# Kernel optimization log

Hardware: AMD Instinct MI355X
Metric: run time of the kernel (lower is better)

The kernel has to match this reference:

```python
import jax, jax.numpy as jnp
import numpy as np

B, N, C = 4, 32768, 64
D_IN = B * C          # 256 == in_channels * batch_size
D_MODEL = 256
HEADS = 2
NUM_EDGES = 4096
N_INC = 131072
EPS = 1e-5
NEG = 0.2


def _leaky(v):
    return jnp.where(v >= 0, v, NEG * v)


def _bn(v, g, b, m, var):  # BatchNorm1d, eval mode (running stats)
    return g * (v - m) * jax.lax.rsqrt(var + EPS) + b


def setup_inputs() -> dict:
    key = jax.random.key(0)
    ks = jax.random.split(key, 16)

    def lin_init(k, fan_in, shape):
        lim = 1.0 / np.sqrt(fan_in)
        return jax.random.uniform(k, shape, jnp.float32, -lim, lim)

    x = jax.random.normal(ks[0], (B, N, C), jnp.float32)
    row_n = jax.random.randint(ks[1], (N_INC,), 0, N, jnp.int32)
    row_e = jax.random.randint(ks[2], (N_INC,), 0, NUM_EDGES, jnp.int32)
    row_e = row_e.at[0].set(NUM_EDGES - 1)  # guarantee max edge id -> num_edges
    hyperedge_all = jnp.stack([row_n, row_e])

    return {
        "x": x,
        "hyperedge_all": hyperedge_all,
        # linear1: d_in -> d_model
        "W1": lin_init(ks[3], D_IN, (D_MODEL, D_IN)),
        "b1": lin_init(ks[4], D_IN, (D_MODEL,)),
        "bn1_g": 1.0 + 0.1 * jax.random.normal(ks[5], (D_MODEL,), jnp.float32),
        "bn1_b": 0.1 * jax.random.normal(ks[6], (D_MODEL,), jnp.float32),
        "bn1_m": 0.01 * jax.random.normal(ks[7], (D_MODEL,), jnp.float32),
        "bn1_v": jnp.ones((D_MODEL,), jnp.float32),
        # HypergraphConv lin: d_model -> heads*d_model (no bias); att: [heads, 2*d_model]
        "attW": lin_init(ks[8], D_MODEL, (HEADS * D_MODEL, D_MODEL)),
        "att": 0.1 * jax.random.normal(ks[9], (HEADS, 2 * D_MODEL), jnp.float32),
        "cb": 0.01 * jax.random.normal(ks[10], (D_MODEL,), jnp.float32),
        "bn2_g": 1.0 + 0.1 * jax.random.normal(ks[11], (D_MODEL,), jnp.float32),
        "bn2_b": 0.1 * jax.random.normal(ks[12], (D_MODEL,), jnp.float32),
        "bn2_m": 0.01 * jax.random.normal(ks[13], (D_MODEL,), jnp.float32),
        "bn2_v": jnp.ones((D_MODEL,), jnp.float32),
        # linear2: d_model -> d_in
        "W2": lin_init(ks[14], D_MODEL, (D_IN, D_MODEL)),
        "b2": lin_init(ks[15], D_MODEL, (D_IN,)),
        "ln_g": jnp.ones((C,), jnp.float32),
        "ln_b": jnp.zeros((C,), jnp.float32),
    }


def reference(x, hyperedge_all, W1, b1, bn1_g, bn1_b, bn1_m, bn1_v,
              attW, att, cb, bn2_g, bn2_b, bn2_m, bn2_v, W2, b2, ln_g, ln_b):
    src = x
    h = x.reshape(N, B * C)                               # [N, D_IN] (raw row-major reshape, as torch)
    h = _leaky(h @ W1.T + b1)                             # [N, D_MODEL]
    h = _bn(h, bn1_g, bn1_b, bn1_m, bn1_v)

    idx_n = hyperedge_all[0]                              # [I] node index per incidence
    idx_e = hyperedge_all[1]                              # [I] hyperedge index per incidence

    # hyperedge_attr = A^T h where A is the (0/1, duplicate-summed) incidence matrix
    eattr = jax.ops.segment_sum(h[idx_n], idx_e, NUM_EDGES)            # [E, D_MODEL]

    # --- HypergraphConv with attention, concat=False ---
    xh = (h @ attW.T).reshape(N, HEADS, D_MODEL)                       # [N, H, D]
    ea = (eattr @ attW.T).reshape(NUM_EDGES, HEADS, D_MODEL)           # [E, H, D]
    att_n, att_e = att[:, :D_MODEL], att[:, D_MODEL:]                  # [H, D] each
    sn = jnp.einsum('nhd,hd->nh', xh, att_n)                           # node score
    se = jnp.einsum('ehd,hd->eh', ea, att_e)                           # edge score
    alpha = _leaky(sn[idx_n] + se[idx_e])                              # [I, H]
    # segment softmax over destination nodes (PyG softmax(alpha, hyperedge_index[0]))
    amax = jax.ops.segment_max(alpha, idx_n, N)
    amax = jnp.where(jnp.isfinite(amax), amax, 0.0)
    ex = jnp.exp(alpha - amax[idx_n])
    denom = jax.ops.segment_sum(ex, idx_n, N)
    alpha = ex / (denom[idx_n] + 1e-16)                                # [I, H]

    ones_i = jnp.ones((N_INC,), h.dtype)
    deg_n = jax.ops.segment_sum(ones_i, idx_n, N)                      # D (hyperedge_weight = 1)
    Dinv = jnp.where(deg_n > 0, 1.0 / deg_n, 0.0)
    deg_e = jax.ops.segment_sum(ones_i, idx_e, NUM_EDGES)              # B
    Binv = jnp.where(deg_e > 0, 1.0 / deg_e, 0.0)

    # node -> edge: edge_out[e] = sum_inc B[e] * alpha * xh[n]
    m1 = Binv[idx_e][:, None, None] * alpha[:, :, None] * xh[idx_n]    # [I, H, D]
    edge_out = jax.ops.segment_sum(m1, idx_e, NUM_EDGES)               # [E, H, D]
    # edge -> node: node_out[n] = sum_inc D[n] * alpha * edge_out[e]
    m2 = Dinv[idx_n][:, None, None] * alpha[:, :, None] * edge_out[idx_e]
    node_out = jax.ops.segment_sum(m2, idx_n, N)                       # [N, H, D]
    x2 = node_out.mean(axis=1) + cb                                    # concat=False -> head mean + bias

    h = _bn(h + x2, bn2_g, bn2_b, bn2_m, bn2_v)
    h = _leaky(h @ W2.T + b2)                                          # [N, D_IN]

    y = src + h.reshape(B, N, C)                                       # residual (raw reshape back)
    mu = y.mean(-1, keepdims=True)                                     # LayerNorm over C
    var = jnp.mean((y - mu) ** 2, -1, keepdims=True)
    return ln_g * (y - mu) * jax.lax.rsqrt(var + EPS) + ln_b
```

## Files before the change

kernel.cpp:

```cpp
#include <hip/hip_runtime.h>

#define NN 32768
#define EE 4096
#define NI 131072
#define NEGS 0.2f
#define EPSV 1e-5f

typedef __bf16 bf16;
typedef __bf16 bf16x8 __attribute__((ext_vector_type(8)));
typedef __bf16 bf16x4 __attribute__((ext_vector_type(4)));
typedef float f32x4 __attribute__((ext_vector_type(4)));

#define AS1 __attribute__((address_space(1)))
#define AS3 __attribute__((address_space(3)))

__device__ __forceinline__ void gld16(const void* g, void* l) {
    __builtin_amdgcn_global_load_lds((const AS1 unsigned*)g, (AS3 unsigned*)l, 16, 0, 0);
}

__device__ __forceinline__ void stage_hl(const bf16* WH, const bf16* WL, bf16* sW,
                                         int buf, int kk, int wave, int lane) {
#pragma unroll
    for (int i = 0; i < 4; ++i) {
        size_t goff = (size_t)(wave*64 + lane)*256 + (size_t)kk*32 + i*8;
        size_t lb = (size_t)buf*16384 + (size_t)(i*256 + wave*64)*8;
        gld16(WH + goff, sW + lb);
        gld16(WL + goff, sW + 8192 + lb);
    }
}

__device__ __forceinline__ void stage_w(const bf16* WB, bf16* sW,
                                        int buf, int kk, int wave, int lane) {
#pragma unroll
    for (int i = 0; i < 4; ++i) {
        gld16(WB + (size_t)(wave*64 + lane)*256 + (size_t)kk*32 + i*8,
              sW + (size_t)buf*8192 + (size_t)(i*256 + wave*64)*8);
    }
}

constexpr size_t OFF_FLAGS = 0;
constexpr size_t OFF_W1F   = 32;
constexpr size_t OFF_WAF   = OFF_W1F + 65536;
constexpr size_t OFF_W2F   = OFF_WAF + 131072;
constexpr size_t OFF_SN    = OFF_W2F + 65536;
constexpr size_t OFF_SE    = OFF_SN + (size_t)NN*2;
constexpr size_t OFF_ALPHA = OFF_SE + (size_t)EE*2;
constexpr size_t OFF_DENOM = OFF_ALPHA + (size_t)NI*2;
constexpr size_t OFF_DEGN  = OFF_DENOM + (size_t)NN*2;
constexpr size_t OFF_DEGE  = OFF_DEGN + (size_t)NN;
constexpr size_t OFF_EATTR = OFF_DEGE + (size_t)EE;
constexpr size_t OFF_EOUT  = OFF_EATTR + (size_t)EE*256;
constexpr size_t OFF_H     = OFF_EOUT + (size_t)EE*512;
constexpr size_t OFF_WBA2  = OFF_H + (size_t)NN*256;
constexpr size_t OFF_WN    = OFF_WBA2 + 65536;
constexpr size_t OFF_WE    = OFF_WN + 512;
constexpr size_t OFF_ECOFF = OFF_WE + 512;
constexpr size_t OFF_ECURS = OFF_ECOFF + 4100;
constexpr size_t OFF_ECLIST= OFF_ECURS + (size_t)EE;
constexpr size_t WS_TOTAL  = OFF_ECLIST + (size_t)NI;

__device__ __forceinline__ float leaky(float v) { return v < 0.f ? NEGS * v : v; }

__device__ __forceinline__ float rdv(const void* p, size_t i, int f) {
    return f ? (float)((const bf16*)p)[i] : ((const float*)p)[i];
}

__device__ __forceinline__ void rd_idx(const void* p, int i, int mode, int& n, int& e) {
    if (mode == 0)      { n = ((const int*)p)[i];            e = ((const int*)p)[NI + i]; }
    else if (mode == 2) { n = ((const int*)p)[2*i];          e = ((const int*)p)[2*i + 1]; }
    else if (mode == 1) { n = (int)((const long long*)p)[i]; e = (int)((const long long*)p)[NI + i]; }
    else if (mode == 3) { n = (int)((const float*)p)[i];     e = (int)((const float*)p)[NI + i]; }
    else                { n = 0; e = 0; }
    if ((unsigned)n >= NN) n = 0;
    if ((unsigned)e >= EE) e = 0;
}

__global__ void detect_kernel(const void* p0, const void* p2, const void* p3, const void* p4,
                              const void* p5, const void* p6, const void* p7, const void* p8,
                              const void* p9, const void* p10, const void* p11, const void* p12,
                              const void* p13, const void* p14, const void* p15, const void* p16,
                              const void* p17, const void* p18, int* F) {
    __shared__ int cnt;
    int b = blockIdx.x, t = threadIdx.x;
    const void* ps[19] = {p0, nullptr, p2, p3, p4, p5, p6, p7, p8, p9, p10,
                          p11, p12, p13, p14, p15, p16, p17, p18};
    const int scan[19] = {2048, 0, 2048, 256, 256, 256, 256, 0, 2048, 1024,
                          256, 256, 256, 256, 0, 256, 256, 0, 0};
    if (b == 1)  { if (t == 0) { F[1] = 1; F[26] = 0; F[27] = 0; F[28] = 0; F[29] = 0; } return; }
    if (b == 18) { if (t == 0) F[18] = 1; return; }
    if (b == 7 || b == 14 || b == 17) {
        if (t == 0) F[b] = (*(const unsigned*)ps[b] == 0x3F803F80u) ? 1 : 0;
        return;
    }
    if (t == 0) cnt = 0;
    __syncthreads();
    int n = scan[b];
    int local = 0;
    for (int i = t; i < n; i += 256) {
        unsigned short u = ((const unsigned short*)ps[b])[i];
        if (((u >> 7) & 0xFFu) >= 0xC0u) local = 1;
    }
    if (local) atomicAdd(&cnt, 1);
    __syncthreads();
    if (t == 0) F[b] = (cnt == 0) ? 1 : 0;
}

__global__ void k_setflags(int* F) {
    if (threadIdx.x == 0) {
        F[25] = (!F[26]) ? 0 : (!F[28]) ? 2 : (!F[27]) ? 1 : (!F[29]) ? 3 : 99;
        int a = 1;
        const int ids[18] = {0,2,3,4,5,6,7,8,9,10,11,12,13,14,15,16,17,18};
        for (int k = 0; k < 18; ++k) a &= F[ids[k]];
        F[20] = a;
    }
}

__global__ void k_idxcheck(const void* p, int* F) {
    int i = blockIdx.x * 256 + threadIdx.x;
    const int*       p32 = (const int*)p;
    const long long* p64 = (const long long*)p;
    const float*     pf  = (const float*)p;
    int n0 = p32[i], e0 = p32[NI + i];
    if ((unsigned)n0 >= NN || (unsigned)e0 >= EE) atomicOr(&F[26], 1);
    int n2 = p32[2*i], e2 = p32[2*i + 1];
    if ((unsigned)n2 >= NN || (unsigned)e2 >= EE) atomicOr(&F[28], 1);
    long long n1 = p64[i], e1 = p64[NI + i];
    if (n1 < 0 || n1 >= NN || e1 < 0 || e1 >= EE) atomicOr(&F[27], 1);
    float nf = pf[i], ef = pf[NI + i];
    if (!(nf >= 0.f && nf < (float)NN && nf == floorf(nf)) ||
        !(ef >= 0.f && ef < (float)EE && ef == floorf(ef))) atomicOr(&F[29], 1);
}

__global__ void marker_kernel(float* OUT, int code) {
    size_t i = (size_t)blockIdx.x * 256 + threadIdx.x;
    OUT[i] = (i == 1) ? (float)code : 0.f;
}

__global__ void convb_kernel(const void* src, bf16* dst, const int* F, int fidx) {
    size_t i = ((size_t)blockIdx.x * 256 + threadIdx.x) * 4;
    if (F[fidx]) {
        *(bf16x4*)(dst + i) = *(const bf16x4*)((const bf16*)src + i);
    } else {
        f32x4 v = *(const f32x4*)((const float*)src + i);
        bf16x4 o;
        o[0] = (bf16)v[0]; o[1] = (bf16)v[1]; o[2] = (bf16)v[2]; o[3] = (bf16)v[3];
        *(bf16x4*)(dst + i) = o;
    }
}

__global__ void k_w1conv(const void* W1, const int* F, bf16* WH, bf16* WL) {
    size_t i = (size_t)blockIdx.x * 256 + threadIdx.x;
    float w = rdv(W1, i, F[2]);
    bf16 h = (bf16)w;
    WH[i] = h;
    WL[i] = (bf16)(w - (float)h);
}

__global__ void k_prep2(const void* g2, const void* be2, const void* m2, const void* v2,
                        const void* cb, const int* F, float* ST) {
    int k = threadIdx.x;
    float s = rdv(g2, k, F[11]) * rsqrtf(rdv(v2, k, F[14]) + EPSV);
    float t = s * (rdv(cb, k, F[10]) - rdv(m2, k, F[13])) + rdv(be2, k, F[12]);
    ST[k] = s; ST[256 + k] = t;
}

__global__ void k_w2conv(const void* W2, const void* b2, const float* ST, const int* F,
                         bf16* WH, bf16* WL, float* B2P) {
    __shared__ float sacc[4];
    int c = blockIdx.x, k = threadIdx.x;
    float w  = rdv(W2, (size_t)c*256 + k, F[15]);
    float sw = ST[k] * w;
    bf16 h = (bf16)sw;
    WH[(size_t)c*256 + k] = h;
    WL[(size_t)c*256 + k] = (bf16)(sw - (float)h);
    float p = ST[256 + k] * w;
#pragma unroll
    for (int m = 32; m >= 1; m >>= 1) p += __shfl_xor(p, m, 64);
    int lane = k & 63, wv = k >> 6;
    if (lane == 0) sacc[wv] = p;
    __syncthreads();
    if (k == 0) B2P[c] = rdv(b2, c, F[16]) + sacc[0] + sacc[1] + sacc[2] + sacc[3];
}

__global__ void k_fold(const void* attW, const void* att, const int* F,
                       float* WN, float* WE) {
    int c = threadIdx.x;
    int h = blockIdx.y;
    int d0 = blockIdx.x * 16;
    int faw = F[8], fat = F[9];
    float swn = 0.f, swe = 0.f;
#pragma unroll 4
    for (int dd = 0; dd < 16; ++dd) {
        int d = d0 + dd;
        float w = rdv(attW, (size_t)(h*256 + d)*256 + c, faw);
        swn += w * rdv(att, h*512 + d, fat);
        swe += w * rdv(att, h*512 + 256 + d, fat);
    }
    atomicAdd(&WN[h*256 + c], swn);
    atomicAdd(&WE[h*256 + c], swe);
}

__global__ void k_deg(const void* __restrict__ idx, float* __restrict__ DEGN,
                      float* __restrict__ DEGE, const int* __restrict__ F) {
    int i = blockIdx.x * 256 + threadIdx.x;
    int n, e; rd_idx(idx, i, F[25], n, e);
    atomicAdd(&DEGN[n], 1.f);
    atomicAdd(&DEGE[e], 1.f);
}

__global__ void scan_a(const float* __restrict__ DEG, int* __restrict__ BSUM) {
    __shared__ int ws[4];
    int b = blockIdx.x, t = threadIdx.x, lane = t & 63, wave = t >> 6;
    f32x4 v = *(const f32x4*)(DEG + ((size_t)b*256 + t)*4);
    int s = (int)v[0] + (int)v[1] + (int)v[2] + (int)v[3];
#pragma unroll
    for (int m = 32; m >= 1; m >>= 1) s += __shfl_xor(s, m, 64);
    if (lane == 0) ws[wave] = s;
    __syncthreads();
    if (t == 0) BSUM[b] = ws[0] + ws[1] + ws[2] + ws[3];
}

__global__ void scan_b2(int* BSN, int* BSE) {
    if (threadIdx.x == 0) { int run = 0; for (int i = 0; i < 32; ++i) { int s = BSN[i]; BSN[i] = run; run += s; } }
    if (threadIdx.x == 1) { int run = 0; for (int i = 0; i < 4;  ++i) { int s = BSE[i]; BSE[i] = run; run += s; } }
}

__global__ void scan_c(float* __restrict__ DEG, const int* __restrict__ BSUM,
                       int* __restrict__ OFF, int* __restrict__ CURS, int total) {
    __shared__ int ws[4];
    int b = blockIdx.x, t = threadIdx.x, lane = t & 63, wave = t >> 6;
    f32x4 v = *(const f32x4*)(DEG + ((size_t)b*256 + t)*4);
    int c0 = (int)v[0], c1 = (int)v[1], c2 = (int)v[2], c3 = (int)v[3];
    int s = c0 + c1 + c2 + c3;
    int p = s;
#pragma unroll
    for (int off = 1; off < 64; off <<= 1) {
        int u = __shfl_up(p, off, 64);
        if (lane >= off) p += u;
    }
    if (lane == 63) ws[wave] = p;
    __syncthreads();
    int wb = 0;
    for (int w = 0; w < wave; ++w) wb += ws[w];
    int run = BSUM[b] + wb + p - s;
    int i0 = (b*256 + t)*4;
    int cs[4] = {c0, c1, c2, c3};
#pragma unroll
    for (int j = 0; j < 4; ++j) {
        OFF[i0 + j] = run; CURS[i0 + j] = run; run += cs[j];
        DEG[i0 + j] = cs[j] > 0 ? 1.f / (float)cs[j] : 0.f;
    }
    if (i0 + 4 == total) OFF[total] = run;
}

__global__ __launch_bounds__(256) void k_h_mfma(const void* __restrict__ x,
                                                const bf16* __restrict__ WH,
                                                const bf16* __restrict__ WL,
                                                const void* b1, const void* g1, const void* be1,
                                                const void* m1, const void* v1,
                                                const float* __restrict__ WN,
                                                const int* __restrict__ F,
                                                float* __restrict__ H,
                                                float* __restrict__ SN) {
    __shared__ float sB[256], sA[256], sM[256], sBE[256], sWN0[256], sWN1[256];
    __shared__ __align__(16) bf16 sW[32768];
    int tid = threadIdx.x;
    {
        sB[tid]  = rdv(b1, tid, F[3]);
        sA[tid]  = rdv(g1, tid, F[4]) * rsqrtf(rdv(v1, tid, F[7]) + EPSV);
        sM[tid]  = rdv(m1, tid, F[6]);
        sBE[tid] = rdv(be1, tid, F[5]);
        sWN0[tid] = WN[tid];
        sWN1[tid] = WN[256 + tid];
    }
    int lane = tid & 63, wave = tid >> 6;
    int l15 = lane & 15, quad = lane >> 4;
    int row0 = (blockIdx.x * 4 + wave) * 16;
    int fx = F[0];
    const size_t abase = (size_t)(row0 + l15) * 256;
    f32x4 acc[16];
#pragma unroll
    for (int t = 0; t < 16; ++t) acc[t] = (f32x4){0.f, 0.f, 0.f, 0.f};
    stage_hl(WH, WL, sW, 0, 0, wave, lane);
    bf16x8 aNb; f32x4 aN0, aN1;
    if (fx) {
        aNb = *(const bf16x8*)((const bf16*)x + abase + quad*8);
    } else {
        aN0 = *(const f32x4*)((const float*)x + abase + quad*8);
        aN1 = *(const f32x4*)((const float*)x + abase + quad*8 + 4);
    }
    __syncthreads();
    int cur = 0;
    for (int kk = 0; kk < 8; ++kk) {
        if (kk < 7) stage_hl(WH, WL, sW, cur ^ 1, kk + 1, wave, lane);
        bf16x8 ah, al;
        if (fx) {
            ah = aNb;
            if (kk < 7) aNb = *(const bf16x8*)((const bf16*)x + abase + (kk+1)*32 + quad*8);
        } else {
            f32x4 a0 = aN0, a1 = aN1;
            if (kk < 7) {
                aN0 = *(const f32x4*)((const float*)x + abase + (kk+1)*32 + quad*8);
                aN1 = *(const f32x4*)((const float*)x + abase + (kk+1)*32 + quad*8 + 4);
            }
#pragma unroll
            for (int j = 0; j < 4; ++j) {
                bf16 h0 = (bf16)a0[j]; ah[j] = h0; al[j] = (bf16)(a0[j] - (float)h0);
                bf16 h1 = (bf16)a1[j]; ah[4+j] = h1; al[4+j] = (bf16)(a1[j] - (float)h1);
            }
        }
        const bf16* pH = sW + cur*16384 + quad*2048 + l15*8;
        const bf16* pL = pH + 8192;
#pragma unroll
        for (int t = 0; t < 16; ++t) {
            bf16x8 bh = *(const bf16x8*)(pH + t*128);
            bf16x8 bl = *(const bf16x8*)(pL + t*128);
            acc[t] = __builtin_amdgcn_mfma_f32_16x16x32_bf16(ah, bh, acc[t], 0, 0, 0);
            if (!fx) acc[t] = __builtin_amdgcn_mfma_f32_16x16x32_bf16(al, bh, acc[t], 0, 0, 0);
            acc[t] = __builtin_amdgcn_mfma_f32_16x16x32_bf16(ah, bl, acc[t], 0, 0, 0);
        }
        __syncthreads();
        cur ^= 1;
    }
    float p0[4] = {0.f, 0.f, 0.f, 0.f}, p1[4] = {0.f, 0.f, 0.f, 0.f};
#pragma unroll
    for (int t = 0; t < 16; ++t) {
        int cc = t*16 + l15;
        float A = sA[cc], Mv = sM[cc], BE = sBE[cc], Bv = sB[cc];
        float w0 = sWN0[cc], w1 = sWN1[cc];
#pragma unroll
        for (int r = 0; r < 4; ++r) {
            int rr = row0 + quad*4 + r;
            float v = leaky(acc[t][r] + Bv);
            float hv = A * (v - Mv) + BE;
            H[(size_t)rr*256 + cc] = hv;
            p0[r] += hv * w0;
            p1[r] += hv * w1;
        }
    }
#pragma unroll
    for (int r = 0; r < 4; ++r) {
#pragma unroll
        for (int m = 8; m >= 1; m >>= 1) {
            p0[r] += __shfl_xor(p0[r], m, 64);
            p1[r] += __shfl_xor(p1[r], m, 64);
        }
        if (l15 == 0) {
            int rr = row0 + quad*4 + r;
            SN[(size_t)rr*2]     = p0[r];
            SN[(size_t)rr*2 + 1] = p1[r];
        }
    }
}

__global__ __launch_bounds__(256) void k_eattrg(const int* __restrict__ COFF,
                                                const int* __restrict__ CLIST,
                                                const void* __restrict__ idx,
                                                const float* __restrict__ H,
                                                const float* __restrict__ WE,
                                                float* __restrict__ SE,
                                                const int* __restrict__ F) {
    __shared__ int s_n[128];
    __shared__ float sq0[4], sq1[4];
    int e = blockIdx.x, t = threadIdx.x;
    int beg = COFF[e], end = COFF[e + 1];
    float acc = 0.f;
    for (int base = beg; base < end; base += 128) {
        int cnt = min(128, end - base);
        if (t < cnt) {
            int i = CLIST[base + t];
            int n, ee; rd_idx(idx, i, F[25], n, ee);
            s_n[t] = n;
        }
        __syncthreads();
        for (int k = 0; k < cnt; ++k) acc += H[(size_t)s_n[k]*256 + t];
        __syncthreads();
    }
    float q0 = acc * WE[t], q1 = acc * WE[256 + t];
    int lane = t & 63, wave = t >> 6;
#pragma unroll
    for (int m = 32; m >= 1; m >>= 1) { q0 += __shfl_xor(q0, m, 64); q1 += __shfl_xor(q1, m, 64); }
    if (lane == 0) { sq0[wave] = q0; sq1[wave] = q1; }
    __syncthreads();
    if (t == 0) {
        SE[(size_t)e*2]     = sq0[0] + sq0[1] + sq0[2] + sq0[3];
        SE[(size_t)e*2 + 1] = sq1[0] + sq1[1] + sq1[2] + sq1[3];
    }
}

__global__ void k_alpha(const void* idx, const float* SN, const float* SE,
                        float* ALPHA, float* DENOM, const int* F) {
    int i = blockIdx.x * 256 + threadIdx.x;
    int n, e; rd_idx(idx, i, F[25], n, e);
    float e0 = expf(leaky(SN[(size_t)n*2]     + SE[(size_t)e*2]));
    float e1 = expf(leaky(SN[(size_t)n*2 + 1] + SE[(size_t)e*2 + 1]));
    ALPHA[(size_t)i*2] = e0; ALPHA[(size_t)i*2 + 1] = e1;
    atomicAdd(&DENOM[(size_t)n*2], e0);
    atomicAdd(&DENOM[(size_t)n*2 + 1], e1);
}

__global__ void fill_e_k(const void* __restrict__ idx, int* __restrict__ CURS,
                         int* __restrict__ CLIST, const int* __restrict__ F) {
    int i = blockIdx.x * 256 + threadIdx.x;
    int n, e; rd_idx(idx, i, F[25], n, e);
    int pos = atomicAdd(&CURS[e], 1);
    CLIST[pos] = i;
}

__global__ void fill_n_k(const void* __restrict__ idx, int* __restrict__ NCURS,
                         int* __restrict__ CLIST, const int* __restrict__ F) {
    int i = blockIdx.x * 256 + threadIdx.x;
    int n, e; rd_idx(idx, i, F[25], n, e);
    int pos = atomicAdd(&NCURS[n], 1);
    CLIST[pos] = i;
}

__global__ __launch_bounds__(256) void m1g_csr_k(const int* __restrict__ COFF,
                                                 const int* __restrict__ CLIST,
                                                 const void* __restrict__ idx,
                                                 const float* __restrict__ ALPHA,
                                                 const float* __restrict__ DENOM,
                                                 const float* __restrict__ H,
                                                 float* __restrict__ G,
                                                 const int* __restrict__ F) {
    __shared__ int   s_n[64];
    __shared__ float s_c0[64];
    __shared__ float s_c1[64];
    int e = blockIdx.x, t = threadIdx.x;
    int beg = COFF[e], end = COFF[e + 1];
    float acc0 = 0.f, acc1 = 0.f;
    for (int base = beg; base < end; base += 64) {
        int cnt = min(64, end - base);
        if (t < cnt) {
            int i = CLIST[base + t];
            int n, ee; rd_idx(idx, i, F[25], n, ee);
            s_n[t]  = n;
            s_c0[t] = ALPHA[(size_t)i*2]     / (DENOM[(size_t)n*2]     + 1e-16f);
            s_c1[t] = ALPHA[(size_t)i*2 + 1] / (DENOM[(size_t)n*2 + 1] + 1e-16f);
        }
        __syncthreads();
        for (int k = 0; k < cnt; ++k) {
            float hv = H[(size_t)s_n[k]*256 + t];
            acc0 += s_c0[k] * hv;
            acc1 += s_c1[k] * hv;
        }
        __syncthreads();
    }
    G[(size_t)e*512 + t]       = acc0;
    G[(size_t)e*512 + 256 + t] = acc1;
}

__global__ __launch_bounds__(256) void gemm_eout_k(const float* __restrict__ G,
                                                   const bf16* __restrict__ WBA,
                                                   const float* __restrict__ BINV,
                                                   float* __restrict__ EOUT) {
    __shared__ __align__(16) bf16 sW[16384];
    int h = blockIdx.y;
    int tid = threadIdx.x, lane = tid & 63, wave = tid >> 6;
    int l15 = lane & 15, quad = lane >> 4;
    int row0 = blockIdx.x * 16;
    const float* Arow = G + (size_t)(row0 + l15) * 512 + h * 256;
    const bf16* WB = WBA + (size_t)h * 65536;
    f32x4 acc[4];
#pragma unroll
    for (int t = 0; t < 4; ++t) acc[t] = (f32x4){0.f, 0.f, 0.f, 0.f};
    stage_w(WB, sW, 0, 0, wave, lane);
    f32x4 aN0 = *(const f32x4*)(Arow + quad*8);
    f32x4 aN1 = *(const f32x4*)(Arow + quad*8 + 4);
    __syncthreads();
    int cur = 0;
    for (int kk = 0; kk < 8; ++kk) {
        if (kk < 7) stage_w(WB, sW, cur ^ 1, kk + 1, wave, lane);
        f32x4 a0 = aN0, a1 = aN1;
        if (kk < 7) {
            aN0 = *(const f32x4*)(Arow + (kk+1)*32 + quad*8);
            aN1 = *(const f32x4*)(Arow + (kk+1)*32 + quad*8 + 4);
        }
        bf16x8 a;
#pragma unroll
        for (int j = 0; j < 4; ++j) { a[j] = (bf16)a0[j]; a[4+j] = (bf16)a1[j]; }
        const bf16* pB = sW + cur*8192 + quad*2048 + l15*8;
#pragma unroll
        for (int tc = 0; tc < 4; ++tc) {
            int t = wave*4 + tc;
            bf16x8 b = *(const bf16x8*)(pB + t*128);
            acc[tc] = __builtin_amdgcn_mfma_f32_16x16x32_bf16(a, b, acc[tc], 0, 0, 0);
        }
        __syncthreads();
        cur ^= 1;
    }
#pragma unroll
    for (int tc = 0; tc < 4; ++tc) {
        int cc = (wave*4 + tc)*16 + l15;
#pragma unroll
        for (int r = 0; r < 4; ++r) {
            int e = row0 + quad*4 + r;
            EOUT[(size_t)e*512 + h*256 + cc] = acc[tc][r] * BINV[e];
        }
    }
}

__global__ __launch_bounds__(256) void k_m2g(const int* __restrict__ NOFF,
                                             const int* __restrict__ CLIST,
                                             const void* __restrict__ idx,
                                             const float* __restrict__ ALPHA,
                                             const float* __restrict__ DENOM,
                                             const float* __restrict__ DINV,
                                             const float* __restrict__ EOUT,
                                             float* __restrict__ H,
                                             const int* __restrict__ F) {
    __shared__ int   s_e[64];
    __shared__ float s_a0[64];
    __shared__ float s_a1[64];
    int n = blockIdx.x, t = threadIdx.x;
    int beg = NOFF[n], end = NOFF[n + 1];
    float dn0 = DENOM[(size_t)n*2]     + 1e-16f;
    float dn1 = DENOM[(size_t)n*2 + 1] + 1e-16f;
    float acc = 0.f;
    for (int base = beg; base < end; base += 64) {
        int cnt = min(64, end - base);
        if (t < cnt) {
            int i = CLIST[base + t];
            int nn, e; rd_idx(idx, i, F[25], nn, e);
            s_e[t]  = e;
            s_a0[t] = ALPHA[(size_t)i*2]     / dn0;
            s_a1[t] = ALPHA[(size_t)i*2 + 1] / dn1;
        }
        __syncthreads();
        for (int k = 0; k < cnt; ++k) {
            int e = s_e[k];
            acc += s_a0[k] * EOUT[(size_t)e*512 + t] + s_a1[k] * EOUT[(size_t)e*512 + 256 + t];
        }
        __syncthreads();
    }
    H[(size_t)n*256 + t] += 0.5f * DINV[n] * acc;
}

__global__ __launch_bounds__(256) void k_out_mfma(const float* __restrict__ H,
                                                  const bf16* __restrict__ WH,
                                                  const bf16* __restrict__ WL,
                                                  const float* __restrict__ B2P,
                                                  const void* __restrict__ x,
                                                  const void* lng, const void* lnb,
                                                  const int* __restrict__ F,
                                                  void* __restrict__ OUT) {
    __shared__ float sB2[256];
    __shared__ float sG[64], sBnd[64];
    __shared__ __align__(16) bf16 sW[32768];
    int tid = threadIdx.x;
    {
        sB2[tid] = B2P[tid];
        if (tid < 64) { sG[tid] = rdv(lng, tid, F[17]); sBnd[tid] = rdv(lnb, tid, F[18]); }
    }
    int lane = tid & 63, wave = tid >> 6;
    int l15 = lane & 15, quad = lane >> 4;
    int row0 = (blockIdx.x * 4 + wave) * 16;
    int fx = F[0], fo = F[20];
    const float* Arow = H + (size_t)(row0 + l15) * 256;
    f32x4 acc[16];
#pragma unroll
    for (int t = 0; t < 16; ++t) acc[t] = (f32x4){0.f, 0.f, 0.f, 0.f};
    stage_hl(WH, WL, sW, 0, 0, wave, lane);
    f32x4 aN0 = *(const f32x4*)(Arow + quad*8);
    f32x4 aN1 = *(const f32x4*)(Arow + quad*8 + 4);
    __syncthreads();
    int cur = 0;
    for (int kk = 0; kk < 8; ++kk) {
        if (kk < 7) stage_hl(WH, WL, sW, cur ^ 1, kk + 1, wave, lane);
        f32x4 a0 = aN0, a1 = aN1;
        if (kk < 7) {
            aN0 = *(const f32x4*)(Arow + (kk+1)*32 + quad*8);
            aN1 = *(const f32x4*)(Arow + (kk+1)*32 + quad*8 + 4);
        }
        bf16x8 ah, al;
#pragma unroll
        for (int j = 0; j < 4; ++j) {
            bf16 h0 = (bf16)a0[j]; ah[j] = h0; al[j] = (bf16)(a0[j] - (float)h0);
            bf16 h1 = (bf16)a1[j]; ah[4+j] = h1; al[4+j] = (bf16)(a1[j] - (float)h1);
        }
        const bf16* pH = sW + cur*16384 + quad*2048 + l15*8;
        const bf16* pL = pH + 8192;
#pragma unroll
        for (int t = 0; t < 16; ++t) {
            bf16x8 bh = *(const bf16x8*)(pH + t*128);
            bf16x8 bl = *(const bf16x8*)(pL + t*128);
            acc[t] = __builtin_amdgcn_mfma_f32_16x16x32_bf16(ah, bh, acc[t], 0, 0, 0);
            acc[t] = __builtin_amdgcn_mfma_f32_16x16x32_bf16(al, bh, acc[t], 0, 0, 0);
            acc[t] = __builtin_amdgcn_mfma_f32_16x16x32_bf16(ah, bl, acc[t], 0, 0, 0);
        }
        __syncthreads();
        cur ^= 1;
    }
#pragma unroll
    for (int t = 0; t < 16; ++t) {
        int cc = t*16 + l15;
        float Bv = sB2[cc];
#pragma unroll
        for (int r = 0; r < 4; ++r) {
            int rr = row0 + quad*4 + r;
            acc[t][r] = rdv(x, (size_t)rr*256 + cc, fx) + leaky(acc[t][r] + Bv);
        }
    }
#pragma unroll
    for (int r = 0; r < 4; ++r) {
        int rr = row0 + quad*4 + r;
#pragma unroll
        for (int g = 0; g < 4; ++g) {
            float s = acc[4*g][r] + acc[4*g+1][r] + acc[4*g+2][r] + acc[4*g+3][r];
            s += __shfl_xor(s, 1, 64); s += __shfl_xor(s, 2, 64);
            s += __shfl_xor(s, 4, 64); s += __shfl_xor(s, 8, 64);
            float mu = s * (1.f / 64.f);
            float q = 0.f;
#pragma unroll
            for (int j = 0; j < 4; ++j) { float d = acc[4*g+j][r] - mu; q += d * d; }
            q += __shfl_xor(q, 1, 64); q += __shfl_xor(q, 2, 64);
            q += __shfl_xor(q, 4, 64); q += __shfl_xor(q, 8, 64);
            float rsq = rsqrtf(q * (1.f / 64.f) + EPSV);
#pragma unroll
            for (int j = 0; j < 4; ++j) {
                int cc = (4*g + j)*16 + l15;
                int gi = cc & 63;
                float o = sG[gi] * (acc[4*g+j][r] - mu) * rsq + sBnd[gi];
                size_t idx = (size_t)rr*256 + cc;
                if (fo) ((bf16*)OUT)[idx] = (bf16)o;
                else    ((float*)OUT)[idx] = o;
            }
        }
    }
}

extern "C" void kernel_launch(void* const* d_in, const int* in_sizes, int n_in,
                              void* d_out, int out_size, void* d_ws, size_t ws_size,
                              hipStream_t stream) {
    float* ws = (float*)d_ws;
    int* F = (int*)(ws + OFF_FLAGS);

    if (ws_size < WS_TOTAL * sizeof(float)) {
        marker_kernel<<<NN, 256, 0, stream>>>((float*)d_out, 300);
        return;
    }
    if (n_in < 19) {
        marker_kernel<<<NN, 256, 0, stream>>>((float*)d_out, 355);
        return;
    }
    const int exp_sizes[19] = {8388608, 262144, 65536, 256, 256, 256, 256, 256, 131072,
                               1024, 256, 256, 256, 256, 256, 65536, 256, 64, 64};
    for (int i = 0; i < 19; ++i) {
        if (in_sizes[i] != exp_sizes[i]) {
            marker_kernel<<<NN, 256, 0, stream>>>((float*)d_out, 330 + i);
            return;
        }
    }

    float* ST    = ws + OFF_W1F;
    float* B2P   = ws + OFF_W1F + 512;
    int*   BSN   = (int*)(ws + OFF_W1F + 768);
    int*   BSE   = BSN + 32;
    int*   NCURS = (int*)(ws + OFF_W1F + 1024);
    int*   NOFF  = (int*)(ws + OFF_W2F);
    bf16*  W1H = (bf16*)(ws + OFF_WAF);
    bf16*  W1L = (bf16*)(ws + OFF_WAF + 32768);
    bf16*  W2H = (bf16*)(ws + OFF_WAF + 65536);
    bf16*  W2L = (bf16*)(ws + OFF_WAF + 98304);
    int*   ECOFF  = (int*)(ws + OFF_ECOFF);
    int*   ECURS  = (int*)(ws + OFF_ECURS);
    int*   CLIST  = (int*)(ws + OFF_ECLIST);

    hipMemsetAsync((char*)d_ws + OFF_DENOM * 4, 0, (OFF_EATTR - OFF_DENOM) * 4, stream);
    hipMemsetAsync((char*)d_ws + OFF_WN * 4, 0, 1024 * 4, stream);

    detect_kernel<<<19, 256, 0, stream>>>(d_in[0], d_in[2], d_in[3], d_in[4], d_in[5], d_in[6],
                                          d_in[7], d_in[8], d_in[9], d_in[10], d_in[11], d_in[12],
                                          d_in[13], d_in[14], d_in[15], d_in[16], d_in[17], d_in[18], F);
    k_idxcheck<<<NI/256, 256, 0, stream>>>(d_in[1], F);
    k_setflags<<<1, 64, 0, stream>>>(F);

    k_deg<<<NI/256, 256, 0, stream>>>(d_in[1], ws + OFF_DEGN, ws + OFF_DEGE, F);
    scan_a<<<32, 256, 0, stream>>>(ws + OFF_DEGN, BSN);
    scan_a<<<4, 256, 0, stream>>>(ws + OFF_DEGE, BSE);
    scan_b2<<<1, 64, 0, stream>>>(BSN, BSE);
    scan_c<<<32, 256, 0, stream>>>(ws + OFF_DEGN, BSN, NOFF, NCURS, NN);
    scan_c<<<4, 256, 0, stream>>>(ws + OFF_DEGE, BSE, ECOFF, ECURS, EE);
    fill_e_k<<<NI/256, 256, 0, stream>>>(d_in[1], ECURS, CLIST, F);

    k_w1conv<<<256, 256, 0, stream>>>(d_in[2], F, W1H, W1L);
    convb_kernel<<<128, 256, 0, stream>>>(d_in[8], (bf16*)(ws + OFF_WBA2), F, 8);
    k_fold<<<dim3(16, 2), 256, 0, stream>>>(d_in[8], d_in[9], F, ws + OFF_WN, ws + OFF_WE);
    k_prep2<<<1, 256, 0, stream>>>(d_in[11], d_in[12], d_in[13], d_in[14], d_in[10], F, ST);
    k_w2conv<<<256, 256, 0, stream>>>(d_in[15], d_in[16], ST, F, W2H, W2L, B2P);

    k_h_mfma<<<NN/64, 256, 0, stream>>>(d_in[0], W1H, W1L, d_in[3], d_in[4], d_in[5],
                                        d_in[6], d_in[7], ws + OFF_WN, F,
                                        ws + OFF_H, ws + OFF_SN);
    k_eattrg<<<EE, 256, 0, stream>>>(ECOFF, CLIST, d_in[1], ws + OFF_H, ws + OFF_WE,
                                     ws + OFF_SE, F);
    k_alpha<<<NI/256, 256, 0, stream>>>(d_in[1], ws + OFF_SN, ws + OFF_SE, ws + OFF_ALPHA,
                                        ws + OFF_DENOM, F);

    m1g_csr_k<<<EE, 256, 0, stream>>>(ECOFF, CLIST, d_in[1], ws + OFF_ALPHA, ws + OFF_DENOM,
                                      ws + OFF_H, ws + OFF_EOUT, F);

    fill_n_k<<<NI/256, 256, 0, stream>>>(d_in[1], NCURS, CLIST, F);

    gemm_eout_k<<<dim3(EE/16, 2), 256, 0, stream>>>(ws + OFF_EOUT, (const bf16*)(ws + OFF_WBA2),
                                                    ws + OFF_DEGE, ws + OFF_EOUT);

    k_m2g<<<NN, 256, 0, stream>>>(NOFF, CLIST, d_in[1], ws + OFF_ALPHA, ws + OFF_DENOM,
                                  ws + OFF_DEGN, ws + OFF_EOUT, ws + OFF_H, F);
    k_out_mfma<<<NN/64, 256, 0, stream>>>(ws + OFF_H, W2H, W2L, B2P, d_in[0],
                                          d_in[17], d_in[18], F, d_out);
}
```

Before: 474.9 us.

## Fold edge-attention projection into node GEMM epilogue and merge scan launches

Per-node dot products with the edge attention weights are now computed in the first GEMM epilogue, and edge scores are built with atomics over incidences (linearity of sum). This replaces the per-edge gather over H rows. Node CSR filling is folded into the alpha kernel, and the node and edge scan kernels are merged into single launches. The cost is extra atomics and a changed memset range. Float atomic order makes the results nondeterministic.

```diff
diff --git a/kernel.cpp b/kernel.cpp
--- a/kernel.cpp
+++ b/kernel.cpp
@@ -208,28 +208,37 @@
     atomicAdd(&DEGE[e], 1.f);
 }
 
-__global__ void scan_a(const float* __restrict__ DEG, int* __restrict__ BSUM) {
-    __shared__ int ws[4];
+__global__ void scan_a(const float* __restrict__ DEGN, const float* __restrict__ DEGE,
+                       int* __restrict__ BS) {
+    __shared__ int wsum[4];
     int b = blockIdx.x, t = threadIdx.x, lane = t & 63, wave = t >> 6;
-    f32x4 v = *(const f32x4*)(DEG + ((size_t)b*256 + t)*4);
+    const float* DEG = (b < 32) ? DEGN + (size_t)b*1024 : DEGE + (size_t)(b-32)*1024;
+    f32x4 v = *(const f32x4*)(DEG + (size_t)t*4);
     int s = (int)v[0] + (int)v[1] + (int)v[2] + (int)v[3];
 #pragma unroll
     for (int m = 32; m >= 1; m >>= 1) s += __shfl_xor(s, m, 64);
-    if (lane == 0) ws[wave] = s;
-    __syncthreads();
-    if (t == 0) BSUM[b] = ws[0] + ws[1] + ws[2] + ws[3];
-}
-
-__global__ void scan_b2(int* BSN, int* BSE) {
-    if (threadIdx.x == 0) { int run = 0; for (int i = 0; i < 32; ++i) { int s = BSN[i]; BSN[i] = run; run += s; } }
-    if (threadIdx.x == 1) { int run = 0; for (int i = 0; i < 4;  ++i) { int s = BSE[i]; BSE[i] = run; run += s; } }
-}
-
-__global__ void scan_c(float* __restrict__ DEG, const int* __restrict__ BSUM,
-                       int* __restrict__ OFF, int* __restrict__ CURS, int total) {
-    __shared__ int ws[4];
+    if (lane == 0) wsum[wave] = s;
+    __syncthreads();
+    if (t == 0) BS[b] = wsum[0] + wsum[1] + wsum[2] + wsum[3];
+}
+
+__global__ void scan_b2(int* BS) {
+    if (threadIdx.x == 0) { int run = 0; for (int i = 0;  i < 32; ++i) { int s = BS[i]; BS[i] = run; run += s; } }
+    if (threadIdx.x == 1) { int run = 0; for (int i = 32; i < 36; ++i) { int s = BS[i]; BS[i] = run; run += s; } }
+}
+
+__global__ void scan_c(float* __restrict__ DEGN, float* __restrict__ DEGE,
+                       const int* __restrict__ BS,
+                       int* __restrict__ NOFF, int* __restrict__ NCURS,
+                       int* __restrict__ ECOFF, int* __restrict__ ECURS) {
+    __shared__ int wsum[4];
     int b = blockIdx.x, t = threadIdx.x, lane = t & 63, wave = t >> 6;
-    f32x4 v = *(const f32x4*)(DEG + ((size_t)b*256 + t)*4);
+    bool isN = (b < 32);
+    int bb = isN ? b : b - 32;
+    float* DEG = isN ? DEGN + (size_t)bb*1024 : DEGE + (size_t)bb*1024;
+    int* OFF   = isN ? NOFF + bb*1024 : ECOFF + bb*1024;
+    int* CURS  = isN ? NCURS + bb*1024 : ECURS + bb*1024;
+    f32x4 v = *(const f32x4*)(DEG + (size_t)t*4);
     int c0 = (int)v[0], c1 = (int)v[1], c2 = (int)v[2], c3 = (int)v[3];
     int s = c0 + c1 + c2 + c3;
     int p = s;
@@ -238,19 +247,19 @@
         int u = __shfl_up(p, off, 64);
         if (lane >= off) p += u;
     }
-    if (lane == 63) ws[wave] = p;
+    if (lane == 63) wsum[wave] = p;
     __syncthreads();
     int wb = 0;
-    for (int w = 0; w < wave; ++w) wb += ws[w];
-    int run = BSUM[b] + wb + p - s;
-    int i0 = (b*256 + t)*4;
+    for (int w = 0; w < wave; ++w) wb += wsum[w];
+    int run = BS[b] + wb + p - s;
+    int i0 = t*4;
     int cs[4] = {c0, c1, c2, c3};
 #pragma unroll
     for (int j = 0; j < 4; ++j) {
         OFF[i0 + j] = run; CURS[i0 + j] = run; run += cs[j];
         DEG[i0 + j] = cs[j] > 0 ? 1.f / (float)cs[j] : 0.f;
     }
-    if (i0 + 4 == total) OFF[total] = run;
+    if (t == 255 && (b == 31 || b == 35)) OFF[1024] = run;
 }
 
 __global__ __launch_bounds__(256) void k_h_mfma(const void* __restrict__ x,
@@ -259,10 +268,13 @@
                                                 const void* b1, const void* g1, const void* be1,
                                                 const void* m1, const void* v1,
                                                 const float* __restrict__ WN,
+                                                const float* __restrict__ WE,
                                                 const int* __restrict__ F,
                                                 float* __restrict__ H,
-                                                float* __restrict__ SN) {
-    __shared__ float sB[256], sA[256], sM[256], sBE[256], sWN0[256], sWN1[256];
+                                                float* __restrict__ SN,
+                                                float* __restrict__ HE) {
+    __shared__ float sB[256], sA[256], sM[256], sBE[256];
+    __shared__ float sWN0[256], sWN1[256], sWE0[256], sWE1[256];
     __shared__ __align__(16) bf16 sW[32768];
     int tid = threadIdx.x;
     {
@@ -272,6 +284,8 @@
         sBE[tid] = rdv(be1, tid, F[5]);
         sWN0[tid] = WN[tid];
         sWN1[tid] = WN[256 + tid];
+        sWE0[tid] = WE[tid];
+        sWE1[tid] = WE[256 + tid];
     }
     int lane = tid & 63, wave = tid >> 6;
     int l15 = lane & 15, quad = lane >> 4;
@@ -322,20 +336,23 @@
         __syncthreads();
         cur ^= 1;
     }
-    float p0[4] = {0.f, 0.f, 0.f, 0.f}, p1[4] = {0.f, 0.f, 0.f, 0.f};
+    float p0[4] = {0.f,0.f,0.f,0.f}, p1[4] = {0.f,0.f,0.f,0.f};
+    float q0[4] = {0.f,0.f,0.f,0.f}, q1[4] = {0.f,0.f,0.f,0.f};
 #pragma unroll
     for (int t = 0; t < 16; ++t) {
         int cc = t*16 + l15;
         float A = sA[cc], Mv = sM[cc], BE = sBE[cc], Bv = sB[cc];
-        float w0 = sWN0[cc], w1 = sWN1[cc];
+        float wn0 = sWN0[cc], wn1 = sWN1[cc], we0 = sWE0[cc], we1 = sWE1[cc];
 #pragma unroll
         for (int r = 0; r < 4; ++r) {
             int rr = row0 + quad*4 + r;
             float v = leaky(acc[t][r] + Bv);
             float hv = A * (v - Mv) + BE;
             H[(size_t)rr*256 + cc] = hv;
-            p0[r] += hv * w0;
-            p1[r] += hv * w1;
+            p0[r] += hv * wn0;
+            p1[r] += hv * wn1;
+            q0[r] += hv * we0;
+            q1[r] += hv * we1;
         }
     }
 #pragma unroll
@@ -344,52 +361,29 @@
         for (int m = 8; m >= 1; m >>= 1) {
             p0[r] += __shfl_xor(p0[r], m, 64);
             p1[r] += __shfl_xor(p1[r], m, 64);
+            q0[r] += __shfl_xor(q0[r], m, 64);
+            q1[r] += __shfl_xor(q1[r], m, 64);
         }
         if (l15 == 0) {
             int rr = row0 + quad*4 + r;
             SN[(size_t)rr*2]     = p0[r];
             SN[(size_t)rr*2 + 1] = p1[r];
-        }
-    }
-}
-
-__global__ __launch_bounds__(256) void k_eattrg(const int* __restrict__ COFF,
-                                                const int* __restrict__ CLIST,
-                                                const void* __restrict__ idx,
-                                                const float* __restrict__ H,
-                                                const float* __restrict__ WE,
-                                                float* __restrict__ SE,
-                                                const int* __restrict__ F) {
-    __shared__ int s_n[128];
-    __shared__ float sq0[4], sq1[4];
-    int e = blockIdx.x, t = threadIdx.x;
-    int beg = COFF[e], end = COFF[e + 1];
-    float acc = 0.f;
-    for (int base = beg; base < end; base += 128) {
-        int cnt = min(128, end - base);
-        if (t < cnt) {
-            int i = CLIST[base + t];
-            int n, ee; rd_idx(idx, i, F[25], n, ee);
-            s_n[t] = n;
-        }
-        __syncthreads();
-        for (int k = 0; k < cnt; ++k) acc += H[(size_t)s_n[k]*256 + t];
-        __syncthreads();
-    }
-    float q0 = acc * WE[t], q1 = acc * WE[256 + t];
-    int lane = t & 63, wave = t >> 6;
-#pragma unroll
-    for (int m = 32; m >= 1; m >>= 1) { q0 += __shfl_xor(q0, m, 64); q1 += __shfl_xor(q1, m, 64); }
-    if (lane == 0) { sq0[wave] = q0; sq1[wave] = q1; }
-    __syncthreads();
-    if (t == 0) {
-        SE[(size_t)e*2]     = sq0[0] + sq0[1] + sq0[2] + sq0[3];
-        SE[(size_t)e*2 + 1] = sq1[0] + sq1[1] + sq1[2] + sq1[3];
-    }
+            HE[(size_t)rr*2]     = q0[r];
+            HE[(size_t)rr*2 + 1] = q1[r];
+        }
+    }
+}
+
+__global__ void k_se(const void* __restrict__ idx, const float* __restrict__ HE,
+                     float* __restrict__ SE, const int* __restrict__ F) {
+    int i = blockIdx.x * 256 + threadIdx.x;
+    int n, e; rd_idx(idx, i, F[25], n, e);
+    atomicAdd(&SE[(size_t)e*2],     HE[(size_t)n*2]);
+    atomicAdd(&SE[(size_t)e*2 + 1], HE[(size_t)n*2 + 1]);
 }
 
 __global__ void k_alpha(const void* idx, const float* SN, const float* SE,
-                        float* ALPHA, float* DENOM, const int* F) {
+                        float* ALPHA, float* DENOM, int* NCURS, int* NLIST, const int* F) {
     int i = blockIdx.x * 256 + threadIdx.x;
     int n, e; rd_idx(idx, i, F[25], n, e);
     float e0 = expf(leaky(SN[(size_t)n*2]     + SE[(size_t)e*2]));
@@ -397,6 +391,8 @@
     ALPHA[(size_t)i*2] = e0; ALPHA[(size_t)i*2 + 1] = e1;
     atomicAdd(&DENOM[(size_t)n*2], e0);
     atomicAdd(&DENOM[(size_t)n*2 + 1], e1);
+    int pos = atomicAdd(&NCURS[n], 1);
+    NLIST[pos] = i;
 }
 
 __global__ void fill_e_k(const void* __restrict__ idx, int* __restrict__ CURS,
@@ -404,14 +400,6 @@
     int i = blockIdx.x * 256 + threadIdx.x;
     int n, e; rd_idx(idx, i, F[25], n, e);
     int pos = atomicAdd(&CURS[e], 1);
-    CLIST[pos] = i;
-}
-
-__global__ void fill_n_k(const void* __restrict__ idx, int* __restrict__ NCURS,
-                         int* __restrict__ CLIST, const int* __restrict__ F) {
-    int i = blockIdx.x * 256 + threadIdx.x;
-    int n, e; rd_idx(idx, i, F[25], n, e);
-    int pos = atomicAdd(&NCURS[n], 1);
     CLIST[pos] = i;
 }
 
@@ -501,7 +489,7 @@
 }
 
 __global__ __launch_bounds__(256) void k_m2g(const int* __restrict__ NOFF,
-                                             const int* __restrict__ CLIST,
+                                             const int* __restrict__ NLIST,
                                              const void* __restrict__ idx,
                                              const float* __restrict__ ALPHA,
                                              const float* __restrict__ DENOM,
@@ -520,7 +508,7 @@
     for (int base = beg; base < end; base += 64) {
         int cnt = min(64, end - base);
         if (t < cnt) {
-            int i = CLIST[base + t];
+            int i = NLIST[base + t];
             int nn, e; rd_idx(idx, i, F[25], nn, e);
             s_e[t]  = e;
             s_a0[t] = ALPHA[(size_t)i*2]     / dn0;
@@ -654,8 +642,7 @@
 
     float* ST    = ws + OFF_W1F;
     float* B2P   = ws + OFF_W1F + 512;
-    int*   BSN   = (int*)(ws + OFF_W1F + 768);
-    int*   BSE   = BSN + 32;
+    int*   BS    = (int*)(ws + OFF_W1F + 768);
     int*   NCURS = (int*)(ws + OFF_W1F + 1024);
     int*   NOFF  = (int*)(ws + OFF_W2F);
     bf16*  W1H = (bf16*)(ws + OFF_WAF);
@@ -665,8 +652,10 @@
     int*   ECOFF  = (int*)(ws + OFF_ECOFF);
     int*   ECURS  = (int*)(ws + OFF_ECURS);
     int*   CLIST  = (int*)(ws + OFF_ECLIST);
-
-    hipMemsetAsync((char*)d_ws + OFF_DENOM * 4, 0, (OFF_EATTR - OFF_DENOM) * 4, stream);
+    float* HE     = ws + OFF_EATTR;
+    int*   NLIST  = (int*)(ws + OFF_EATTR + 65536);
+
+    hipMemsetAsync((char*)d_ws + OFF_SE * 4, 0, (OFF_EATTR - OFF_SE) * 4, stream);
     hipMemsetAsync((char*)d_ws + OFF_WN * 4, 0, 1024 * 4, stream);
 
     detect_kernel<<<19, 256, 0, stream>>>(d_in[0], d_in[2], d_in[3], d_in[4], d_in[5], d_in[6],
@@ -676,11 +665,9 @@
     k_setflags<<<1, 64, 0, stream>>>(F);
 
     k_deg<<<NI/256, 256, 0, stream>>>(d_in[1], ws + OFF_DEGN, ws + OFF_DEGE, F);
-    scan_a<<<32, 256, 0, stream>>>(ws + OFF_DEGN, BSN);
-    scan_a<<<4, 256, 0, stream>>>(ws + OFF_DEGE, BSE);
-    scan_b2<<<1, 64, 0, stream>>>(BSN, BSE);
-    scan_c<<<32, 256, 0, stream>>>(ws + OFF_DEGN, BSN, NOFF, NCURS, NN);
-    scan_c<<<4, 256, 0, stream>>>(ws + OFF_DEGE, BSE, ECOFF, ECURS, EE);
+    scan_a<<<36, 256, 0, stream>>>(ws + OFF_DEGN, ws + OFF_DEGE, BS);
+    scan_b2<<<1, 64, 0, stream>>>(BS);
+    scan_c<<<36, 256, 0, stream>>>(ws + OFF_DEGN, ws + OFF_DEGE, BS, NOFF, NCURS, ECOFF, ECURS);
     fill_e_k<<<NI/256, 256, 0, stream>>>(d_in[1], ECURS, CLIST, F);
 
     k_w1conv<<<256, 256, 0, stream>>>(d_in[2], F, W1H, W1L);
@@ -690,22 +677,19 @@
     k_w2conv<<<256, 256, 0, stream>>>(d_in[15], d_in[16], ST, F, W2H, W2L, B2P);
 
     k_h_mfma<<<NN/64, 256, 0, stream>>>(d_in[0], W1H, W1L, d_in[3], d_in[4], d_in[5],
-                                        d_in[6], d_in[7], ws + OFF_WN, F,
-                                        ws + OFF_H, ws + OFF_SN);
-    k_eattrg<<<EE, 256, 0, stream>>>(ECOFF, CLIST, d_in[1], ws + OFF_H, ws + OFF_WE,
-                                     ws + OFF_SE, F);
+                                        d_in[6], d_in[7], ws + OFF_WN, ws + OFF_WE, F,
+                                        ws + OFF_H, ws + OFF_SN, HE);
+    k_se<<<NI/256, 256, 0, stream>>>(d_in[1], HE, ws + OFF_SE, F);
     k_alpha<<<NI/256, 256, 0, stream>>>(d_in[1], ws + OFF_SN, ws + OFF_SE, ws + OFF_ALPHA,
-                                        ws + OFF_DENOM, F);
+                                        ws + OFF_DENOM, NCURS, NLIST, F);
 
     m1g_csr_k<<<EE, 256, 0, stream>>>(ECOFF, CLIST, d_in[1], ws + OFF_ALPHA, ws + OFF_DENOM,
                                       ws + OFF_H, ws + OFF_EOUT, F);
 
-    fill_n_k<<<NI/256, 256, 0, stream>>>(d_in[1], NCURS, CLIST, F);
-
     gemm_eout_k<<<dim3(EE/16, 2), 256, 0, stream>>>(ws + OFF_EOUT, (const bf16*)(ws + OFF_WBA2),
                                                     ws + OFF_DEGE, ws + OFF_EOUT);
 
-    k_m2g<<<NN, 256, 0, stream>>>(NOFF, CLIST, d_in[1], ws + OFF_ALPHA, ws + OFF_DENOM,
+    k_m2g<<<NN, 256, 0, stream>>>(NOFF, NLIST, d_in[1], ws + OFF_ALPHA, ws + OFF_DENOM,
                                   ws + OFF_DEGN, ws + OFF_EOUT, ws + OFF_H, F);
     k_out_mfma<<<NN/64, 256, 0, stream>>>(ws + OFF_H, W2H, W2L, B2P, d_in[0],
                                           d_in[17], d_in[18], F, d_out);
```

Result: no change. 471.8 us (-0.7%).
